# Performance work log

Measured on AMD Instinct MI355X. Metric: run time of the kernel, lower is better.

The kernel has to match this reference:

```python
import jax, jax.numpy as jnp
import numpy as np

N_ATOMS = 8192
N_BONDS = 8192


def setup_inputs() -> dict:
    key = jax.random.key(0)
    k = jax.random.split(key, 7)
    N, B = N_ATOMS, N_BONDS
    # atom coordinates, spread out so min pairwise distance stays away from 0
    x = jax.random.normal(k[0], (N, 3), dtype=jnp.float32) * 10.0
    # bonded pairs; guarantee i != j so bond distances are strictly positive
    src = jax.random.randint(k[1], (B,), 0, N)
    off = jax.random.randint(k[2], (B,), 1, N)
    dst = (src + off) % N
    pairs = jnp.stack([src, dst], axis=1).astype(jnp.int64)
    kb = jax.random.uniform(k[3], (B,), dtype=jnp.float32, minval=100.0, maxval=400.0)
    b0 = jax.random.uniform(k[4], (B,), dtype=jnp.float32, minval=1.0, maxval=2.0)
    eps_ij = jax.random.uniform(k[5], (N, N), dtype=jnp.float32, minval=0.0, maxval=0.2)
    rmin_ij = jax.random.uniform(k[6], (N, N), dtype=jnp.float32, minval=2.0, maxval=4.0)
    # symmetrize like the torch initialize() (outer-product / outer-sum forms)
    eps_ij = 0.5 * (eps_ij + eps_ij.T)
    rmin_ij = 0.5 * (rmin_ij + rmin_ij.T)
    return {"x": x, "pairs": pairs, "kb": kb, "b0": b0,
            "eps_ij": eps_ij, "rmin_ij": rmin_ij}


def reference(x, pairs, kb, b0, eps_ij, rmin_ij):
    # --- harmonic bond term: V_bond = sum kb * (|x_i - x_j| - b0)^2 ---
    dvec = x[pairs[:, 0]] - x[pairs[:, 1]]            # [B,3]
    dis = jnp.sqrt(jnp.sum(dvec * dvec, axis=1))      # [B]
    V_bond = jnp.sum(kb * (dis - b0) ** 2)

    # --- all-pairs Lennard-Jones term ---
    N = x.shape[0]
    sq = jnp.sum(x * x, axis=1)                       # [N]
    d2 = sq[:, None] + sq[None, :] - 2.0 * (x @ x.T)  # [N,N] squared distances
    d2 = jnp.maximum(d2, 0.0)
    # safe sqrt (diagonal is exactly 0); diagonal then gets +1 from eye,
    # matching torch.cdist(x,x) + torch.eye(N)
    dist = jnp.where(d2 > 0, jnp.sqrt(jnp.where(d2 > 0, d2, 1.0)), 0.0)
    dist = dist + jnp.eye(N, dtype=x.dtype)
    rod = rmin_ij / dist
    r6 = rod ** 6
    vdw = eps_ij * (r6 * r6 - 2.0 * r6)               # eps*(rod^12 - 2*rod^6)
    # sum over strict upper triangle (i < j)
    V_vdw = jnp.sum(jnp.triu(vdw, k=1))

    return V_bond + V_vdw
```

## Files before the change

### kernel.cpp

```cpp
#include <hip/hip_runtime.h>

#define NA 8192
#define NB 8192

__global__ void pack_x_kernel(const float* __restrict__ x, float4* __restrict__ x4, int n) {
    int t = blockIdx.x * blockDim.x + threadIdx.x;
    if (t < n) {
        float a = x[3 * t + 0], b = x[3 * t + 1], c = x[3 * t + 2];
        float sq = __fadd_rn(__fadd_rn(__fmul_rn(a, a), __fmul_rn(b, b)), __fmul_rn(c, c));
        x4[t] = make_float4(a, b, c, sq);
    }
}

__device__ __forceinline__ void block_reduce_atomic(float v, float* __restrict__ out) {
#pragma unroll
    for (int off = 32; off > 0; off >>= 1) v += __shfl_down(v, off);
    __shared__ float smem[8];
    const int lane = threadIdx.x & 63;
    const int wave = threadIdx.x >> 6;
    if (lane == 0) smem[wave] = v;
    __syncthreads();
    if (threadIdx.x == 0) {
        float s = 0.0f;
        const int nw = (int)(blockDim.x >> 6);
        for (int w = 0; w < nw; ++w) s += smem[w];
        atomicAdd(out, s);
    }
}

__global__ void bond_kernel(const float* __restrict__ x, const int* __restrict__ pairs,
                            const float* __restrict__ kb, const float* __restrict__ b0,
                            float* __restrict__ out) {
    int t = blockIdx.x * blockDim.x + threadIdx.x;
    float v = 0.0f;
    if (t < NB) {
        int i = pairs[2 * t + 0] & (NA - 1);
        int j = pairs[2 * t + 1] & (NA - 1);
        float dx = __fsub_rn(x[3 * i + 0], x[3 * j + 0]);
        float dy = __fsub_rn(x[3 * i + 1], x[3 * j + 1]);
        float dz = __fsub_rn(x[3 * i + 2], x[3 * j + 2]);
        float ss = __fadd_rn(__fadd_rn(__fmul_rn(dx, dx), __fmul_rn(dy, dy)), __fmul_rn(dz, dz));
        float dis = __fsqrt_rn(ss);
        float d = __fsub_rn(dis, b0[t]);
        v = __fmul_rn(kb[t], __fmul_rn(d, d));
    }
    block_reduce_atomic(v, out);
}

__device__ __forceinline__ float lj_pair(const float4 xi, const float4 xj,
                                         const float e, const float rm) {
    float dot = fmaf(xi.z, xj.z, fmaf(xi.y, xj.y, __fmul_rn(xi.x, xj.x)));
    float t   = __fadd_rn(xi.w, xj.w);
    float d2  = fmaf(-2.0f, dot, t);
    d2 = fmaxf(d2, 0.0f);
    float dist = (d2 > 0.0f) ? __fsqrt_rn(d2) : 0.0f;
    float rod  = __fdiv_rn(rm, dist);
    float r2 = __fmul_rn(rod, rod);
    float r6 = __fmul_rn(__fmul_rn(r2, r2), r2);
    return __fmul_rn(e, __fsub_rn(__fmul_rn(r6, r6), __fmul_rn(2.0f, r6)));
}

__global__ __launch_bounds__(256) void lj_kernel(const float4* __restrict__ x4,
                                                 const float* __restrict__ eps,
                                                 const float* __restrict__ rmin,
                                                 float* __restrict__ out) {
    const int N = NA;
    float acc = 0.0f;
    const int rowA = (int)blockIdx.x;
    const int rowB = N - 1 - rowA;

#pragma unroll
    for (int r = 0; r < 2; ++r) {
        const int i = (r == 0) ? rowA : rowB;
        const float4 xi = x4[i];
        const float* __restrict__ erow = eps + (size_t)i * N;
        const float* __restrict__ rrow = rmin + (size_t)i * N;

        int j = i + 1 + (int)threadIdx.x;
        for (; j + 768 < N; j += 1024) {
            const float4 xj0 = x4[j];
            const float4 xj1 = x4[j + 256];
            const float4 xj2 = x4[j + 512];
            const float4 xj3 = x4[j + 768];
            const float e0 = erow[j],       e1 = erow[j + 256];
            const float e2 = erow[j + 512], e3 = erow[j + 768];
            const float m0 = rrow[j],       m1 = rrow[j + 256];
            const float m2 = rrow[j + 512], m3 = rrow[j + 768];
            float a0 = lj_pair(xi, xj0, e0, m0);
            float a1 = lj_pair(xi, xj1, e1, m1);
            float a2 = lj_pair(xi, xj2, e2, m2);
            float a3 = lj_pair(xi, xj3, e3, m3);
            acc += (a0 + a1) + (a2 + a3);
        }
        for (; j < N; j += 256) {
            acc += lj_pair(xi, x4[j], erow[j], rrow[j]);
        }
    }
    block_reduce_atomic(acc, out);
}

extern "C" void kernel_launch(void* const* d_in, const int* in_sizes, int n_in,
                              void* d_out, int out_size, void* d_ws, size_t ws_size,
                              hipStream_t stream) {
    const float* x     = (const float*)d_in[0];
    const int*   pairs = (const int*)d_in[1];
    const float* kb    = (const float*)d_in[2];
    const float* b0    = (const float*)d_in[3];
    const float* eps   = (const float*)d_in[4];
    const float* rmin  = (const float*)d_in[5];
    float* out = (float*)d_out;
    float4* x4 = (float4*)d_ws;

    hipMemsetAsync(out, 0, sizeof(float), stream);
    pack_x_kernel<<<(NA + 255) / 256, 256, 0, stream>>>(x, x4, NA);
    bond_kernel<<<(NB + 255) / 256, 256, 0, stream>>>(x, pairs, kb, b0, out);
    lj_kernel<<<NA / 2, 256, 0, stream>>>(x4, eps, rmin, out);
}
```

Before: 479.9 us.

## Stage eps/rmin rows through double-buffered LDS with float4 loads

The LJ kernel now loads eps and rmin rows in 2048-element chunks using aligned float4 global loads, staged into double-buffered shared memory. The next chunk is prefetched into registers while the current one is computed. Chunk starts are aligned down to a multiple of four, and entries with j <= i are masked off. The aim is to replace misaligned scalar loads with wide coalesced ones and to overlap memory latency with compute. The cost is extra shared-memory traffic, block-wide barriers and some over-fetch at row boundaries.

```diff
diff --git a/kernel.cpp b/kernel.cpp
--- a/kernel.cpp
+++ b/kernel.cpp
@@ -2,6 +2,7 @@
 
 #define NA 8192
 #define NB 8192
+#define CH 2048
 
 __global__ void pack_x_kernel(const float* __restrict__ x, float4* __restrict__ x4, int n) {
     int t = blockIdx.x * blockDim.x + threadIdx.x;
@@ -65,36 +66,73 @@
                                                  const float* __restrict__ rmin,
                                                  float* __restrict__ out) {
     const int N = NA;
+    __shared__ float se[2][CH];
+    __shared__ float sm[2][CH];
     float acc = 0.0f;
+    const int tid = (int)threadIdx.x;
     const int rowA = (int)blockIdx.x;
-    const int rowB = N - 1 - rowA;
 
-#pragma unroll
+    float4 ea, eb, ma, mb;
+
+#pragma unroll 1
     for (int r = 0; r < 2; ++r) {
-        const int i = (r == 0) ? rowA : rowB;
+        const int i = (r == 0) ? rowA : (N - 1 - rowA);
         const float4 xi = x4[i];
         const float* __restrict__ erow = eps + (size_t)i * N;
         const float* __restrict__ rrow = rmin + (size_t)i * N;
+        const int c0 = (i + 1) & ~3;
+        if (c0 >= N) continue;
 
-        int j = i + 1 + (int)threadIdx.x;
-        for (; j + 768 < N; j += 1024) {
-            const float4 xj0 = x4[j];
-            const float4 xj1 = x4[j + 256];
-            const float4 xj2 = x4[j + 512];
-            const float4 xj3 = x4[j + 768];
-            const float e0 = erow[j],       e1 = erow[j + 256];
-            const float e2 = erow[j + 512], e3 = erow[j + 768];
-            const float m0 = rrow[j],       m1 = rrow[j + 256];
-            const float m2 = rrow[j + 512], m3 = rrow[j + 768];
-            float a0 = lj_pair(xi, xj0, e0, m0);
-            float a1 = lj_pair(xi, xj1, e1, m1);
-            float a2 = lj_pair(xi, xj2, e2, m2);
-            float a3 = lj_pair(xi, xj3, e3, m3);
-            acc += (a0 + a1) + (a2 + a3);
+
+#define LOADCHUNK(cc) do {                                            \
+            const float4* __restrict__ e4 = (const float4*)(erow + (cc)); \
+            const float4* __restrict__ m4 = (const float4*)(rrow + (cc)); \
+            ea = e4[tid]; eb = e4[tid + 256];                          \
+            ma = m4[tid]; mb = m4[tid + 256];                          \
+        } while (0)
+
+#define WRITE_LDS(b) do {                                             \
+            ((float4*)se[b])[tid] = ea; ((float4*)se[b])[tid + 256] = eb; \
+            ((float4*)sm[b])[tid] = ma; ((float4*)sm[b])[tid + 256] = mb; \
+        } while (0)
+
+#define COMPUTE(b, cbase) do {                                        \
+            _Pragma("unroll")                                         \
+            for (int k = 0; k < CH / 256; ++k) {                      \
+                const int j = (cbase) + k * 256 + tid;                \
+                if (j < N) {                                          \
+                    const float e = se[b][k * 256 + tid];             \
+                    const float m = sm[b][k * 256 + tid];             \
+                    const float v = lj_pair(xi, x4[j], e, m);         \
+                    acc += (j > i) ? v : 0.0f;                        \
+                }                                                     \
+            }                                                         \
+        } while (0)
+
+        int c = c0;
+        LOADCHUNK(c);
+        WRITE_LDS(0);
+        int nxt = c + CH;
+        bool havenext = (nxt < N);
+        if (havenext) LOADCHUNK(nxt);
+        __syncthreads();
+        int cur = 0;
+        while (true) {
+            COMPUTE(cur, c);
+            if (!havenext) break;
+            __syncthreads();
+            WRITE_LDS(cur ^ 1);
+            c = nxt;
+            nxt = c + CH;
+            havenext = (nxt < N);
+            if (havenext) LOADCHUNK(nxt);
+            __syncthreads();
+            cur ^= 1;
         }
-        for (; j < N; j += 256) {
-            acc += lj_pair(xi, x4[j], erow[j], rrow[j]);
-        }
+        __syncthreads();
+#undef LOADCHUNK
+#undef WRITE_LDS
+#undef COMPUTE
     }
     block_reduce_atomic(acc, out);
 }
```

New measurement: 495.5 us. +3.2%, slower.
